# Optimization experiments

Hardware: AMD Instinct MI355X
Metric: run time of the kernel (lower is better)

Reference implementation:

```python
import jax, jax.numpy as jnp
import numpy as np

B, S, F = 4, 2048, 1024

def setup_inputs() -> dict:
    key = jax.random.key(0)
    ks = jax.random.split(key, 9)
    s = 1.0 / np.sqrt(F)
    return {
        "q": jax.random.normal(ks[0], (B, S, F), jnp.float32),
        "k": jax.random.normal(ks[1], (B, S, F), jnp.float32),
        "v": jax.random.normal(ks[2], (B, S, F), jnp.float32),
        "Wq": jax.random.normal(ks[3], (F, F), jnp.float32) * s,
        "bq": jax.random.normal(ks[4], (F,), jnp.float32) * s,
        "Wk": jax.random.normal(ks[5], (F, F), jnp.float32) * s,
        "bk": jax.random.normal(ks[6], (F,), jnp.float32) * s,
        "Wv": jax.random.normal(ks[7], (F, F), jnp.float32) * s,
        "bv": jax.random.normal(ks[8], (F,), jnp.float32) * s,
    }

def reference(q, k, v, Wq, bq, Wk, bk, Wv, bv):
    # Linear layers: x @ W^T + b (torch nn.Linear convention)
    qp = jnp.einsum('bsf,gf->bsg', q, Wq) + bq
    kp = jnp.einsum('bsf,gf->bsg', k, Wk) + bk
    vp = jnp.einsum('bsf,gf->bsg', v, Wv) + bv
    # Unscaled attention (no 1/sqrt(d)), as in the original module
    attn = jax.nn.softmax(jnp.einsum('bqf,bkf->bqk', qp, kp), axis=-1)
    return jnp.einsum('bqk,bkf->bqf', attn, vp) + q
```

## Files before the change

### kernel.cpp

```cpp
#include <hip/hip_runtime.h>

typedef unsigned short u16;
typedef __bf16 bf16x8 __attribute__((ext_vector_type(8)));
typedef float f32x4 __attribute__((ext_vector_type(4)));
typedef u16 u16x8 __attribute__((ext_vector_type(8)));

union B8 { u16x8 u; bf16x8 b; };

__device__ __forceinline__ u16 f2b(float f){
  unsigned u = __float_as_uint(f);
  return (u16)((u + 0x7FFFu + ((u >> 16) & 1u)) >> 16);
}
__device__ __forceinline__ float b2f(u16 h){ return __uint_as_float(((unsigned)h) << 16); }

__device__ __forceinline__ void gload16(const u16* g, u16* l){
  __builtin_amdgcn_global_load_lds((const __attribute__((address_space(1))) void*)g,
                                   (__attribute__((address_space(3))) void*)l, 16, 0, 0);
}

__global__ __launch_bounds__(256) void prep_kernel(
    const float* __restrict__ v, const float* __restrict__ Wv,
    const float* __restrict__ Wq, const float* __restrict__ Wk,
    u16* __restrict__ v_b, u16* __restrict__ Wv_b,
    u16* __restrict__ WqT_pair, u16* __restrict__ WkT_pair)
{
  __shared__ float lds[64][65];
  const int blk = blockIdx.x, t = threadIdx.x;
  if (blk < 4608){
    const float* src; u16* dst; long base;
    if (blk < 4096){ src = v;  dst = v_b;  base = blk; }
    else           { src = Wv; dst = Wv_b; base = blk - 4096; }
    long i = base * 256 + t;
    float4 x0 = ((const float4*)src)[2 * i];
    float4 x1 = ((const float4*)src)[2 * i + 1];
    float xs[8] = {x0.x, x0.y, x0.z, x0.w, x1.x, x1.y, x1.z, x1.w};
    u16x8 h;
    #pragma unroll
    for (int j = 0; j < 8; j++) h[j] = f2b(xs[j]);
    ((u16x8*)dst)[i] = h;
  } else {
    int tt = blk - 4608;
    const float* W = (tt >> 8) ? Wk : Wq;
    u16* outp      = (tt >> 8) ? WkT_pair : WqT_pair;
    int t16 = tt & 255, g0 = (t16 >> 4) * 64, f0 = (t16 & 15) * 64;
    int c4 = (t & 15) * 4, r0 = t >> 4;
    #pragma unroll
    for (int it = 0; it < 4; it++){
      int r = r0 + it * 16;
      float4 x = *(const float4*)&W[(long)(g0 + r) * 1024 + f0 + c4];
      lds[r][c4] = x.x; lds[r][c4+1] = x.y; lds[r][c4+2] = x.z; lds[r][c4+3] = x.w;
    }
    __syncthreads();
    #pragma unroll
    for (int it = 0; it < 2; it++){
      int task = t + it * 256;
      int fl = task >> 3, gi = task & 7;
      u16x8 h, l;
      #pragma unroll
      for (int jj = 0; jj < 8; jj++){
        float xv = lds[gi * 8 + jj][fl];
        h[jj] = f2b(xv); l[jj] = f2b(xv - b2f(h[jj]));
      }
      u16* o = outp + (long)(f0 + fl) * 2048 + ((g0 >> 3) + gi) * 16;
      *(u16x8*)o = h;
      *(u16x8*)(o + 8) = l;
    }
  }
}

__global__ __launch_bounds__(256) void bvec_kernel(
    const u16* __restrict__ WkT_pair, const float* __restrict__ bq, float* __restrict__ b)
{
  const int wave = threadIdx.x >> 6, lane = threadIdx.x & 63;
  const int e = blockIdx.x * 4 + wave;
  const u16* row = WkT_pair + (long)e * 2048;
  float acc = 0.f;
  #pragma unroll
  for (int ii = 0; ii < 2; ii++){
    int gi = lane * 2 + ii;
    const u16* p = row + gi * 16;
    #pragma unroll
    for (int j = 0; j < 8; j++)
      acc += (b2f(p[j]) + b2f(p[j + 8])) * bq[gi * 8 + j];
  }
  #pragma unroll
  for (int off = 32; off > 0; off >>= 1) acc += __shfl_xor(acc, off, 64);
  if (lane == 0) b[e] = acc;
}

__global__ __launch_bounds__(256) void split_qk_kernel(
    const float* __restrict__ q, const float* __restrict__ kk,
    const float* __restrict__ b,
    u16* __restrict__ q_pair, u16* __restrict__ k_pair, float* __restrict__ kb)
{
  const int blk = blockIdx.x, t = threadIdx.x;
  const bool isK = blk >= 4096;
  const float* src = isK ? kk : q;
  u16* dst = isK ? k_pair : q_pair;
  long base = isK ? blk - 4096 : blk;
  long i = base * 256 + t;
  float4 x0 = ((const float4*)src)[2 * i];
  float4 x1 = ((const float4*)src)[2 * i + 1];
  float xs[8] = {x0.x, x0.y, x0.z, x0.w, x1.x, x1.y, x1.z, x1.w};
  u16x8 h, l;
  #pragma unroll
  for (int j = 0; j < 8; j++){ h[j] = f2b(xs[j]); l[j] = f2b(xs[j] - b2f(h[j])); }
  ((u16x8*)dst)[2 * i]     = h;
  ((u16x8*)dst)[2 * i + 1] = l;
  if (isK){
    const int f = (t & 127) * 8;
    float d = 0.f;
    #pragma unroll
    for (int j = 0; j < 8; j++) d += xs[j] * b[f + j];
    #pragma unroll
    for (int off = 32; off > 0; off >>= 1) d += __shfl_xor(d, off, 64);
    __shared__ float red[4];
    if ((t & 63) == 0) red[t >> 6] = d;
    __syncthreads();
    if (t == 0)   kb[base * 2]     = red[0] + red[1];
    if (t == 128) kb[base * 2 + 1] = red[2] + red[3];
  }
}

__global__ __launch_bounds__(256) void reduce_split_kernel(
    const float* __restrict__ part, u16* __restrict__ out_pair, long nper)
{
  long i = (long)blockIdx.x * 256 + threadIdx.x;
  float s[8];
  #pragma unroll
  for (int j = 0; j < 8; j++) s[j] = 0.f;
  #pragma unroll
  for (int z = 0; z < 4; z++){
    float4 a0 = ((const float4*)(part + z * nper))[2 * i];
    float4 a1 = ((const float4*)(part + z * nper))[2 * i + 1];
    s[0]+=a0.x; s[1]+=a0.y; s[2]+=a0.z; s[3]+=a0.w;
    s[4]+=a1.x; s[5]+=a1.y; s[6]+=a1.z; s[7]+=a1.w;
  }
  u16x8 h, l;
  #pragma unroll
  for (int j = 0; j < 8; j++){ h[j] = f2b(s[j]); l[j] = f2b(s[j] - b2f(h[j])); }
  long e = (i * 8) >> 10;
  long g = i & 127;
  u16* o = out_pair + e * 2048 + g * 16;
  *(u16x8*)o = h;
  *(u16x8*)(o + 8) = l;
}

__device__ __forceinline__ void xcd_remap(int& tx, int& ty, int& tz){
  const int GX = gridDim.x, GY = gridDim.y;
  int b  = blockIdx.x + GX * (blockIdx.y + GY * blockIdx.z);
  int NB = GX * GY * gridDim.z;
  int rank = (b & 7) * (NB >> 3) + (b >> 3);
  int pz = GX * GY;
  tz = rank / pz;
  int r = rank - tz * pz;
  ty = r / GX;
  tx = r - ty * GX;
}

constexpr int BM = 128, BN = 128, BK = 32;

__device__ __forceinline__ int lds1_idx(int row, int g){ return row * 32 + g * 8; }
__device__ __forceinline__ int lds2_idx(int row, int g){
  return row * 64 + (((g ^ (row & 7)) & 7) << 3);
}

template<bool DUAL, int EPI>
__global__ __launch_bounds__(256, 4)
void gemm_nt(const u16* __restrict__ A, const u16* __restrict__ Bm,
             const float* __restrict__ bias, const float* __restrict__ residual,
             void* __restrict__ out0,
             int M, int N, int K, int Krow,
             long sAb, long sBb, long sOb, long sRb, int seq)
{
  constexpr int RW = DUAL ? 64 : 32;
  __shared__ u16 lds[2][BM * RW];

  int tx, ty, tz; xcd_remap(tx, ty, tz);
  const int t = threadIdx.x;
  const int tileM = ty * BM;
  const int tileN = tx * BN;
  const long rs = DUAL ? 2L * Krow : (long)Krow;

  const u16* gA = A  + tz * sAb + (long)tileM * rs;
  const u16* gB = Bm + tz * sBb + (long)tileN * rs;

  const int wave = t >> 6, lane = t & 63;
  const int wm = (wave >> 1) * 64, wn = (wave & 1) * 64;
  const int lr = lane & 15;
  const int lg = lane >> 4;

  const u16 *pa, *pb;
  long jstride;
  int  ldsbase, ldsstep, nissue, kadv;
  if (DUAL){
    const int lr8 = lane >> 3, sl = lane & 7;
    const int g = sl ^ lr8;
    pa = gA + (long)(wave * 32 + lr8) * rs + g * 8;
    pb = gB + (long)(wave * 32 + lr8) * rs + g * 8;
    jstride = 8 * rs;
    ldsbase = (wave * 32) * 64; ldsstep = 8 * 64;
    nissue = 4; kadv = 64;
  } else {
    pa = gA + (long)(wave * 32 + (lane >> 2)) * rs + (lane & 3) * 8;
    pb = gB + (long)(wave * 32 + (lane >> 2)) * rs + (lane & 3) * 8;
    jstride = 16 * rs;
    ldsbase = (wave * 32) * 32; ldsstep = 16 * 32;
    nissue = 2; kadv = 32;
  }

  f32x4 acc[4][4] = {};

  for (int k0 = 0; k0 < K; k0 += BK){
    __syncthreads();
    #pragma unroll 4
    for (int j = 0; j < nissue; j++){
      gload16(pa + j * jstride, &lds[0][ldsbase + j * ldsstep]);
      gload16(pb + j * jstride, &lds[1][ldsbase + j * ldsstep]);
    }
    pa += kadv; pb += kadv;
    __syncthreads();

    if (DUAL){
      B8 ah[4], al[4], bh[4], bl[4];
      #pragma unroll
      for (int mt = 0; mt < 4; mt++){
        int row = wm + mt * 16 + lr;
        ah[mt].u = *(const u16x8*)&lds[0][lds2_idx(row, lg * 2)];
        al[mt].u = *(const u16x8*)&lds[0][lds2_idx(row, lg * 2 + 1)];
      }
      #pragma unroll
      for (int nt = 0; nt < 4; nt++){
        int row = wn + nt * 16 + lr;
        bh[nt].u = *(const u16x8*)&lds[1][lds2_idx(row, lg * 2)];
        bl[nt].u = *(const u16x8*)&lds[1][lds2_idx(row, lg * 2 + 1)];
      }
      #pragma unroll
      for (int mt = 0; mt < 4; mt++){
        #pragma unroll
        for (int nt = 0; nt < 4; nt++){
          acc[mt][nt] = __builtin_amdgcn_mfma_f32_16x16x32_bf16(ah[mt].b, bh[nt].b, acc[mt][nt], 0, 0, 0);
          acc[mt][nt] = __builtin_amdgcn_mfma_f32_16x16x32_bf16(ah[mt].b, bl[nt].b, acc[mt][nt], 0, 0, 0);
          acc[mt][nt] = __builtin_amdgcn_mfma_f32_16x16x32_bf16(al[mt].b, bh[nt].b, acc[mt][nt], 0, 0, 0);
        }
      }
    } else {
      B8 af[4], bf[4];
      #pragma unroll
      for (int mt = 0; mt < 4; mt++)
        af[mt].u = *(const u16x8*)&lds[0][lds1_idx(wm + mt * 16 + lr, lg)];
      #pragma unroll
      for (int nt = 0; nt < 4; nt++)
        bf[nt].u = *(const u16x8*)&lds[1][lds1_idx(wn + nt * 16 + lr, lg)];
      #pragma unroll
      for (int mt = 0; mt < 4; mt++)
        #pragma unroll
        for (int nt = 0; nt < 4; nt++)
          acc[mt][nt] = __builtin_amdgcn_mfma_f32_16x16x32_bf16(af[mt].b, bf[nt].b, acc[mt][nt], 0, 0, 0);
    }
  }

  const int rq = lg * 4;
  #pragma unroll
  for (int nt = 0; nt < 4; nt++){
    const int n = tileN + wn + nt * 16 + lr;
    float bv = 0.f;
    if (EPI == 0 && bias) bv = bias[n];
    if (EPI == 2 && bias) bv = bias[(long)tz * N + n];
    #pragma unroll
    for (int mt = 0; mt < 4; mt++){
      #pragma unroll
      for (int r = 0; r < 4; r++){
        const int m = tileM + wm + mt * 16 + rq + r;
        float val = acc[mt][nt][r] + bv;
        if (EPI == 0){
          u16 h = f2b(val);
          u16* o = (u16*)out0 + (long)tz * sOb + (long)m * 2 * N + ((n >> 3) << 4) + (n & 7);
          o[0] = h;
          o[8] = f2b(val - b2f(h));
        } else if (EPI == 2){
          ((float*)out0)[(long)tz * sOb + (long)m * N + n] = val;
        } else if (EPI == 3){
          float res = residual[(long)tz * sRb + (long)m * N + n];
          ((float*)out0)[(long)tz * sOb + (long)m * N + n] = val + res;
        } else {
          if (bias) val += bias[m];
          long idx = (long)(n / seq) * ((long)M * seq) + (long)m * seq + (n % seq);
          ((u16*)out0)[idx] = f2b(val);
        }
      }
    }
  }
}

__global__ __launch_bounds__(256)
void softmax_kernel(const float* __restrict__ S, u16* __restrict__ P, int n){
  const long row = blockIdx.x;
  const float* r = S + row * (long)n;
  const int t = threadIdx.x;
  float v[8];
  float mx = -3.0e38f;
  #pragma unroll
  for (int i = 0; i < 8; i++){ v[i] = r[t + (i << 8)]; mx = fmaxf(mx, v[i]); }
  #pragma unroll
  for (int off = 32; off > 0; off >>= 1) mx = fmaxf(mx, __shfl_xor(mx, off, 64));
  __shared__ float red[8];
  const int wave = t >> 6;
  if ((t & 63) == 0) red[wave] = mx;
  __syncthreads();
  mx = fmaxf(fmaxf(red[0], red[1]), fmaxf(red[2], red[3]));
  float s = 0.f;
  #pragma unroll
  for (int i = 0; i < 8; i++){ v[i] = __expf(v[i] - mx); s += v[i]; }
  #pragma unroll
  for (int off = 32; off > 0; off >>= 1) s += __shfl_xor(s, off, 64);
  if ((t & 63) == 0) red[4 + wave] = s;
  __syncthreads();
  s = red[4] + red[5] + red[6] + red[7];
  const float inv = 1.f / s;
  u16* pr = P + row * (long)n;
  #pragma unroll
  for (int i = 0; i < 8; i++) pr[t + (i << 8)] = f2b(v[i] * inv);
}

extern "C" void kernel_launch(void* const* d_in, const int* in_sizes, int n_in,
                              void* d_out, int out_size, void* d_ws, size_t ws_size,
                              hipStream_t stream){
  (void)in_sizes; (void)n_in; (void)out_size; (void)ws_size;
  const float* q  = (const float*)d_in[0];
  const float* k  = (const float*)d_in[1];
  const float* v  = (const float*)d_in[2];
  const float* Wq = (const float*)d_in[3];
  const float* bq = (const float*)d_in[4];
  const float* Wk = (const float*)d_in[5];
  const float* Wv = (const float*)d_in[7];
  const float* bv = (const float*)d_in[8];
  float* out = (float*)d_out;

  const int B = 4, S = 2048, F = 1024;
  const long NSF = (long)B * S * F;
  const long NFF = (long)F * F;
  const long NSS = (long)B * S * S;

  char* w = (char*)d_ws;
  auto alloc = [&](long bytes) -> char* {
    char* p = w; w += (bytes + 255) & ~(long)255; return p;
  };
  u16*   tmp_pair = (u16*)alloc(2 * NSF * 2);
  u16*   k_pair   = (u16*)alloc(2 * NSF * 2);
  u16*   vpT      = (u16*)alloc(NSF * 2);
  float* kb       = (float*)alloc((long)B * S * 4);
  char* zone2 = alloc(NSS * 2 + NSS * 4);
  u16*   attn   = (u16*)zone2;
  float* scores = (float*)(zone2 + NSS * 2);
  u16*   q_pair   = (u16*)zone2;
  char*  z3       = zone2 + NSS * 2;
  u16*   v_b      = (u16*)z3;
  u16*   Wv_b     = (u16*)(z3 + NSF * 2);
  u16*   WqT_pair = (u16*)(z3 + NSF * 2 + NFF * 2);
  u16*   WkT_pair = WqT_pair + 2 * NFF;
  float* b_vec    = (float*)(WkT_pair + 2 * NFF);
  float* Mt_part  = (float*)((char*)b_vec + 4096);
  u16*   Mt_pair  = (u16*)((char*)Mt_part + 4 * NFF * 4);

  dim3 blk(256);

  prep_kernel<<<dim3(5120), blk, 0, stream>>>(
      v, Wv, Wq, Wk, v_b, Wv_b, WqT_pair, WkT_pair);

  bvec_kernel<<<dim3(256), blk, 0, stream>>>(WkT_pair, bq, b_vec);

  gemm_nt<false, 4><<<dim3((B * S) / BN, F / BM, 1), blk, 0, stream>>>(
      Wv_b, v_b, bv, nullptr, vpT,
      F, B * S, F, F, 0, 0, 0, 0, S);

  split_qk_kernel<<<dim3(8192), blk, 0, stream>>>(q, k, b_vec, q_pair, k_pair, kb);

  gemm_nt<true, 2><<<dim3(F / BN, F / BM, 4), blk, 0, stream>>>(
      WkT_pair, WqT_pair, nullptr, nullptr, Mt_part,
      F, F, 256, F, 512, 512, NFF, 0, S);

  reduce_split_kernel<<<dim3(512), blk, 0, stream>>>(Mt_part, Mt_pair, NFF);

  gemm_nt<true, 0><<<dim3(F / BN, (B * S) / BM, 1), blk, 0, stream>>>(
      q_pair, Mt_pair, nullptr, nullptr, tmp_pair,
      B * S, F, F, F, 0, 0, 0, 0, S);

  gemm_nt<true, 2><<<dim3(S / BN, S / BM, B), blk, 0, stream>>>(
      tmp_pair, k_pair, kb, nullptr, scores,
      S, S, F, F, (long)S * 2 * F, (long)S * 2 * F, (long)S * S, 0, S);

  softmax_kernel<<<dim3(B * S), blk, 0, stream>>>(scores, attn, S);

  gemm_nt<false, 3><<<dim3(F / BN, S / BM, B), blk, 0, stream>>>(
      attn, vpT, nullptr, q, out,
      S, F, S, S, (long)S * S, (long)F * S, (long)S * F, (long)S * F, S);
}
```

Baseline: 447.2 us.

## Use 256x256 tiled 512-thread dual-bf16 GEMM for attention scores

Replaces the generic gemm_nt launch for the QK^T scores with a dedicated kernel that uses 256x256 output tiles, 8 waves per block, and double-buffered direct-to-LDS loads. It computes the split-bf16 (hi/lo) product with three MFMAs per fragment pair. The larger tile is meant to raise arithmetic intensity and cut global/LDS traffic per flop. In exchange it uses 128 KB of LDS and large accumulator register usage, which can limit occupancy, and the grid shrinks to 256 blocks.

```diff
diff --git a/kernel.cpp b/kernel.cpp
--- a/kernel.cpp
+++ b/kernel.cpp
@@ -288,6 +288,108 @@
           long idx = (long)(n / seq) * ((long)M * seq) + (long)m * seq + (n % seq);
           ((u16*)out0)[idx] = f2b(val);
         }
+      }
+    }
+  }
+}
+
+__global__ __launch_bounds__(512, 2)
+void gemm_nt256_dual(const u16* __restrict__ A, const u16* __restrict__ Bm,
+                     const float* __restrict__ bias, float* __restrict__ out,
+                     int N, int K, int Krow, long sAb, long sBb, long sOb)
+{
+  __shared__ u16 lds[2][2][256 * 64];
+
+  int tx, ty, tz; xcd_remap(tx, ty, tz);
+  const int t = threadIdx.x;
+  const int wave = t >> 6, lane = t & 63;
+  const int tileM = ty * 256, tileN = tx * 256;
+  const long rs = 2L * Krow;
+
+  const u16* gA = A  + tz * sAb + (long)tileM * rs;
+  const u16* gB = Bm + tz * sBb + (long)tileN * rs;
+
+  const int r8 = lane >> 3, c8 = lane & 7;
+  const u16* pA = gA + (long)(wave * 32 + r8) * rs + (c8 ^ r8) * 8;
+  const u16* pB = gB + (long)(wave * 32 + r8) * rs + (c8 ^ r8) * 8;
+  const int ldsrow = wave * 32;
+
+  const int wm = (wave >> 2) * 128, wn = (wave & 3) * 64;
+  const int lr = lane & 15, lg = lane >> 4;
+
+  f32x4 acc[8][4] = {};
+  const int ntiles = K / 32;
+
+  #pragma unroll
+  for (int j = 0; j < 4; j++){
+    gload16(pA + (long)j * 8 * rs, &lds[0][0][(ldsrow + j * 8) * 64]);
+    gload16(pB + (long)j * 8 * rs, &lds[0][1][(ldsrow + j * 8) * 64]);
+  }
+
+  for (int tt = 0; tt < ntiles; tt++){
+    const int b = tt & 1;
+    if (tt + 1 < ntiles){
+      const long ko = (long)(tt + 1) * 64;
+      #pragma unroll
+      for (int j = 0; j < 4; j++){
+        gload16(pA + ko + (long)j * 8 * rs, &lds[b ^ 1][0][(ldsrow + j * 8) * 64]);
+        gload16(pB + ko + (long)j * 8 * rs, &lds[b ^ 1][1][(ldsrow + j * 8) * 64]);
+      }
+      asm volatile("s_waitcnt vmcnt(8)" ::: "memory");
+    } else {
+      asm volatile("s_waitcnt vmcnt(0)" ::: "memory");
+    }
+    __builtin_amdgcn_sched_barrier(0);
+    __builtin_amdgcn_s_barrier();
+
+    B8 bh[4], bl[4];
+    #pragma unroll
+    for (int p = 0; p < 4; p++){
+      if (p){
+        __builtin_amdgcn_s_barrier();
+      }
+      if (p == 0){
+        #pragma unroll
+        for (int nt = 0; nt < 4; nt++){
+          int row = wn + nt * 16 + lr;
+          bh[nt].u = *(const u16x8*)&lds[b][1][lds2_idx(row, lg * 2)];
+          bl[nt].u = *(const u16x8*)&lds[b][1][lds2_idx(row, lg * 2 + 1)];
+        }
+      }
+      B8 ah[2], al[2];
+      #pragma unroll
+      for (int mm = 0; mm < 2; mm++){
+        int row = wm + (p * 2 + mm) * 16 + lr;
+        ah[mm].u = *(const u16x8*)&lds[b][0][lds2_idx(row, lg * 2)];
+        al[mm].u = *(const u16x8*)&lds[b][0][lds2_idx(row, lg * 2 + 1)];
+      }
+      __builtin_amdgcn_s_setprio(1);
+      #pragma unroll
+      for (int mm = 0; mm < 2; mm++){
+        #pragma unroll
+        for (int nt = 0; nt < 4; nt++){
+          acc[p*2+mm][nt] = __builtin_amdgcn_mfma_f32_16x16x32_bf16(ah[mm].b, bh[nt].b, acc[p*2+mm][nt], 0, 0, 0);
+          acc[p*2+mm][nt] = __builtin_amdgcn_mfma_f32_16x16x32_bf16(ah[mm].b, bl[nt].b, acc[p*2+mm][nt], 0, 0, 0);
+          acc[p*2+mm][nt] = __builtin_amdgcn_mfma_f32_16x16x32_bf16(al[mm].b, bh[nt].b, acc[p*2+mm][nt], 0, 0, 0);
+        }
+      }
+      __builtin_amdgcn_s_setprio(0);
+    }
+    __builtin_amdgcn_sched_barrier(0);
+    __builtin_amdgcn_s_barrier();
+  }
+
+  const int rq = lg * 4;
+  #pragma unroll
+  for (int nt = 0; nt < 4; nt++){
+    const int n = tileN + wn + nt * 16 + lr;
+    const float bv = bias ? bias[(long)tz * N + n] : 0.f;
+    #pragma unroll
+    for (int mt = 0; mt < 8; mt++){
+      #pragma unroll
+      for (int r = 0; r < 4; r++){
+        const int m = tileM + wm + mt * 16 + rq + r;
+        out[(long)tz * sOb + (long)m * N + n] = acc[mt][nt][r] + bv;
       }
     }
   }
@@ -386,9 +488,9 @@
       q_pair, Mt_pair, nullptr, nullptr, tmp_pair,
       B * S, F, F, F, 0, 0, 0, 0, S);
 
-  gemm_nt<true, 2><<<dim3(S / BN, S / BM, B), blk, 0, stream>>>(
-      tmp_pair, k_pair, kb, nullptr, scores,
-      S, S, F, F, (long)S * 2 * F, (long)S * 2 * F, (long)S * S, 0, S);
+  gemm_nt256_dual<<<dim3(S / 256, S / 256, B), dim3(512), 0, stream>>>(
+      tmp_pair, k_pair, kb, scores,
+      S, F, F, (long)S * 2 * F, (long)S * 2 * F, (long)S * S);
 
   softmax_kernel<<<dim3(B * S), blk, 0, stream>>>(scores, attn, S);
 
```

Measured after the change: 446.6 us. No clear change (-0.1%).

## Fuse V-projection and q·Mt GEMMs into one heterogeneous launch

Applied to the files above, without the earlier changes.

Refactors the GEMM into a device body function and adds a combined kernel. Its blocks run either the single-precision-split V projection tile or the dual-bf16 q×Mt tile, chosen by block index with per-XCD rank mapping. This removes one launch and lets the two independent GEMMs share the GPU concurrently, filling tail and underutilization. The shared memory is sized for the larger dual variant, which may lower occupancy for the V-projection blocks.

```diff
diff --git a/kernel.cpp b/kernel.cpp
--- a/kernel.cpp
+++ b/kernel.cpp
@@ -166,17 +166,14 @@
 }
 
 template<bool DUAL, int EPI>
-__global__ __launch_bounds__(256, 4)
-void gemm_nt(const u16* __restrict__ A, const u16* __restrict__ Bm,
-             const float* __restrict__ bias, const float* __restrict__ residual,
-             void* __restrict__ out0,
-             int M, int N, int K, int Krow,
-             long sAb, long sBb, long sOb, long sRb, int seq)
-{
-  constexpr int RW = DUAL ? 64 : 32;
-  __shared__ u16 lds[2][BM * RW];
-
-  int tx, ty, tz; xcd_remap(tx, ty, tz);
+__device__ __forceinline__ void gemm_nt_body(
+    int tx, int ty, int tz, u16* __restrict__ lds0, u16* __restrict__ lds1,
+    const u16* __restrict__ A, const u16* __restrict__ Bm,
+    const float* __restrict__ bias, const float* __restrict__ residual,
+    void* __restrict__ out0,
+    int M, int N, int K, int Krow,
+    long sAb, long sBb, long sOb, long sRb, int seq)
+{
   const int t = threadIdx.x;
   const int tileM = ty * BM;
   const int tileN = tx * BN;
@@ -215,8 +212,8 @@
     __syncthreads();
     #pragma unroll 4
     for (int j = 0; j < nissue; j++){
-      gload16(pa + j * jstride, &lds[0][ldsbase + j * ldsstep]);
-      gload16(pb + j * jstride, &lds[1][ldsbase + j * ldsstep]);
+      gload16(pa + j * jstride, &lds0[ldsbase + j * ldsstep]);
+      gload16(pb + j * jstride, &lds1[ldsbase + j * ldsstep]);
     }
     pa += kadv; pb += kadv;
     __syncthreads();
@@ -226,14 +223,14 @@
       #pragma unroll
       for (int mt = 0; mt < 4; mt++){
         int row = wm + mt * 16 + lr;
-        ah[mt].u = *(const u16x8*)&lds[0][lds2_idx(row, lg * 2)];
-        al[mt].u = *(const u16x8*)&lds[0][lds2_idx(row, lg * 2 + 1)];
+        ah[mt].u = *(const u16x8*)&lds0[lds2_idx(row, lg * 2)];
+        al[mt].u = *(const u16x8*)&lds0[lds2_idx(row, lg * 2 + 1)];
       }
       #pragma unroll
       for (int nt = 0; nt < 4; nt++){
         int row = wn + nt * 16 + lr;
-        bh[nt].u = *(const u16x8*)&lds[1][lds2_idx(row, lg * 2)];
-        bl[nt].u = *(const u16x8*)&lds[1][lds2_idx(row, lg * 2 + 1)];
+        bh[nt].u = *(const u16x8*)&lds1[lds2_idx(row, lg * 2)];
+        bl[nt].u = *(const u16x8*)&lds1[lds2_idx(row, lg * 2 + 1)];
       }
       #pragma unroll
       for (int mt = 0; mt < 4; mt++){
@@ -248,10 +245,10 @@
       B8 af[4], bf[4];
       #pragma unroll
       for (int mt = 0; mt < 4; mt++)
-        af[mt].u = *(const u16x8*)&lds[0][lds1_idx(wm + mt * 16 + lr, lg)];
+        af[mt].u = *(const u16x8*)&lds0[lds1_idx(wm + mt * 16 + lr, lg)];
       #pragma unroll
       for (int nt = 0; nt < 4; nt++)
-        bf[nt].u = *(const u16x8*)&lds[1][lds1_idx(wn + nt * 16 + lr, lg)];
+        bf[nt].u = *(const u16x8*)&lds1[lds1_idx(wn + nt * 16 + lr, lg)];
       #pragma unroll
       for (int mt = 0; mt < 4; mt++)
         #pragma unroll
@@ -293,6 +290,43 @@
   }
 }
 
+template<bool DUAL, int EPI>
+__global__ __launch_bounds__(256, 4)
+void gemm_nt(const u16* __restrict__ A, const u16* __restrict__ Bm,
+             const float* __restrict__ bias, const float* __restrict__ residual,
+             void* __restrict__ out0,
+             int M, int N, int K, int Krow,
+             long sAb, long sBb, long sOb, long sRb, int seq)
+{
+  constexpr int RW = DUAL ? 64 : 32;
+  __shared__ u16 sh[2 * BM * RW];
+  int tx, ty, tz; xcd_remap(tx, ty, tz);
+  gemm_nt_body<DUAL, EPI>(tx, ty, tz, sh, sh + BM * RW,
+                          A, Bm, bias, residual, out0,
+                          M, N, K, Krow, sAb, sBb, sOb, sRb, seq);
+}
+
+__global__ __launch_bounds__(256, 4)
+void gemm_step37(const u16* __restrict__ Wv_b, const u16* __restrict__ v_b,
+                 const float* __restrict__ bv, u16* __restrict__ vpT,
+                 const u16* __restrict__ q_pair, const u16* __restrict__ Mt_pair,
+                 u16* __restrict__ tmp_pair)
+{
+  __shared__ u16 sh[2 * BM * 64];
+  const int b = blockIdx.x, xcd = b & 7, i = b >> 3;
+  if (i < 64){
+    const int rank = xcd * 64 + i;
+    gemm_nt_body<false, 4>(rank & 63, rank >> 6, 0, sh, sh + BM * 32,
+                           Wv_b, v_b, bv, nullptr, vpT,
+                           1024, 8192, 1024, 1024, 0, 0, 0, 0, 2048);
+  } else {
+    const int rank = xcd * 64 + (i - 64);
+    gemm_nt_body<true, 0>(rank & 7, rank >> 3, 0, sh, sh + BM * 64,
+                          q_pair, Mt_pair, nullptr, nullptr, tmp_pair,
+                          8192, 1024, 1024, 1024, 0, 0, 0, 0, 2048);
+  }
+}
+
 __global__ __launch_bounds__(256)
 void softmax_kernel(const float* __restrict__ S, u16* __restrict__ P, int n){
   const long row = blockIdx.x;
@@ -370,10 +404,6 @@
 
   bvec_kernel<<<dim3(256), blk, 0, stream>>>(WkT_pair, bq, b_vec);
 
-  gemm_nt<false, 4><<<dim3((B * S) / BN, F / BM, 1), blk, 0, stream>>>(
-      Wv_b, v_b, bv, nullptr, vpT,
-      F, B * S, F, F, 0, 0, 0, 0, S);
-
   split_qk_kernel<<<dim3(8192), blk, 0, stream>>>(q, k, b_vec, q_pair, k_pair, kb);
 
   gemm_nt<true, 2><<<dim3(F / BN, F / BM, 4), blk, 0, stream>>>(
@@ -382,9 +412,8 @@
 
   reduce_split_kernel<<<dim3(512), blk, 0, stream>>>(Mt_part, Mt_pair, NFF);
 
-  gemm_nt<true, 0><<<dim3(F / BN, (B * S) / BM, 1), blk, 0, stream>>>(
-      q_pair, Mt_pair, nullptr, nullptr, tmp_pair,
-      B * S, F, F, F, 0, 0, 0, 0, S);
+  gemm_step37<<<dim3(1024), blk, 0, stream>>>(
+      Wv_b, v_b, bv, vpT, q_pair, Mt_pair, tmp_pair);
 
   gemm_nt<true, 2><<<dim3(S / BN, S / BM, B), blk, 0, stream>>>(
       tmp_pair, k_pair, kb, nullptr, scores,
```

After: 422.3 us. 1.06x faster.
